# Kernel optimization log

Measured on AMD Instinct MI355X. Metric: run time of the kernel, lower is better.

## Reference

```python
import jax, jax.numpy as jnp
import numpy as np

B, M, D = 64, 256, 256          # batch, tokens, feature dim
A = 18                          # num_actions
E, S = 4, 64                    # num_experts, slots per expert (E*S == M)
H = 512                         # expert hidden size


def setup_inputs() -> dict:
    key = jax.random.key(0)
    ks = jax.random.split(key, 7)
    obs = jax.random.normal(ks[0], (B, M, D), dtype=jnp.float32)
    action = jax.random.randint(ks[1], (B,), 0, A, dtype=jnp.int64)
    # Soft-MoE slot projection phi: [D, E, S]
    phi = jax.random.normal(ks[2], (D, E, S), dtype=jnp.float32) / np.sqrt(D)
    # Per-expert MLP: Dense(H) + relu, then Dense(A*D) output head
    w1 = jax.random.normal(ks[3], (E, D, H), dtype=jnp.float32) * np.sqrt(2.0 / D)
    b1 = jnp.zeros((E, H), dtype=jnp.float32)
    w2 = jax.random.normal(ks[4], (E, H, A * D), dtype=jnp.float32) * np.sqrt(2.0 / H)
    b2 = jnp.zeros((E, A * D), dtype=jnp.float32)
    return {"obs": obs, "action": action, "phi": phi,
            "w1": w1, "b1": b1, "w2": w2, "b2": b2}


def reference(obs, action, phi, w1, b1, w2, b2):
    b, m, d = obs.shape
    # ---- Soft-MoE dispatch / combine (Puigcerver et al.) ----
    logits = jnp.einsum('bmd,des->bmes', obs, phi)            # [b,m,e,s]
    dispatch = jax.nn.softmax(logits, axis=1)                 # softmax over tokens
    combine = jax.nn.softmax(logits.reshape(b, m, E * S), axis=-1)
    combine = combine.reshape(b, m, E, S)                     # softmax over all slots
    slots = jnp.einsum('bmd,bmes->besd', obs, dispatch)       # [b,e,s,d]
    # ---- per-expert MLP: Dense(H)+relu -> Dense(A*d) ----
    h = jax.nn.relu(jnp.einsum('besd,edh->besh', slots, w1) + b1[None, :, None, :])
    y = jnp.einsum('besh,ehk->besk', h, w2) + b2[None, :, None, :]   # k = A*d
    # ---- combine slots back to tokens ----
    out = jnp.einsum('bmes,besk->bmk', combine, y)            # [b,m,A*d]
    # reshape to [b, A, m, d] as in the original module
    out = out.reshape(b, m, A, d).transpose(0, 2, 1, 3)       # [b,A,m,d]
    # ---- one-hot action selection via einsum (as in source) ----
    action_one_hot = jax.nn.one_hot(action, A, dtype=out.dtype)
    logits_out = jnp.einsum('bamd,ba->bmd', out, action_one_hot)
    return logits_out  # logits of the categorical transition distribution
```

## Files before the change

### kernel.cpp

```cpp
#include <hip/hip_runtime.h>

#define B_   64
#define M_   256
#define D_   256
#define A_   18
#define E_   4
#define S_   64
#define ES_  256
#define H_   512
#define K2_  (A_*D_)

typedef _Float16 f16;
typedef _Float16 f16x4 __attribute__((ext_vector_type(4)));
typedef _Float16 f16x8 __attribute__((ext_vector_type(8)));
typedef float    f32x4 __attribute__((ext_vector_type(4)));

static __device__ __forceinline__ f16x8 cat8(f16x4 a, f16x4 b) {
  return __builtin_shufflevector(a, b, 0, 1, 2, 3, 4, 5, 6, 7);
}
static __device__ __forceinline__ f16x8 pack8(float4 u0, float4 u1) {
  f16x8 a;
  a[0] = (f16)u0.x; a[1] = (f16)u0.y; a[2] = (f16)u0.z; a[3] = (f16)u0.w;
  a[4] = (f16)u1.x; a[5] = (f16)u1.y; a[6] = (f16)u1.z; a[7] = (f16)u1.w;
  return a;
}

__global__ __launch_bounds__(256) void k_preplog(
    const float* __restrict__ obs, const float* __restrict__ phi,
    const float* __restrict__ w1, const float* __restrict__ w2,
    const int* __restrict__ action,
    f16* __restrict__ obsT16, f16* __restrict__ w1T, f16* __restrict__ w2T,
    int* __restrict__ order,
    f16* __restrict__ exp16, f16* __restrict__ expT16,
    float* __restrict__ rowpart, float* __restrict__ colpart)
{
  __shared__ f16 Bs[64][264];
  f16 (*T)[68] = reinterpret_cast<f16(*)[68]>(&Bs[0][0]);
  const int bx = blockIdx.x;
  const int t  = threadIdx.x;

  if (bx < 3456) {
    const int rr = t >> 4, cc = (t & 15) * 4;
    const float* src; f16* dst; int R, C, r0, c0;
    if (bx < 1024) {
      const int x = bx & 3, y = (bx >> 2) & 3, z = bx >> 4;
      src = obs + (long)z * (M_ * D_); dst = obsT16 + (long)z * (M_ * D_);
      R = M_; C = D_; r0 = y * 64; c0 = x * 64;
    } else if (bx < 1152) {
      const int idx = bx - 1024;
      const int x = idx & 7, y = (idx >> 3) & 3, z = idx >> 5;
      src = w1 + (long)z * (D_ * H_); dst = w1T + (long)z * (H_ * D_);
      R = D_; C = H_; r0 = y * 64; c0 = x * 64;
    } else {
      const int idx = bx - 1152;
      const int x = idx % 72, rem = idx / 72, y = rem & 7, z = rem >> 3;
      src = w2 + (long)z * ((long)H_ * K2_); dst = w2T + (long)z * ((long)K2_ * H_);
      R = H_; C = K2_; r0 = y * 64; c0 = x * 64;
    }
#pragma unroll
    for (int p = 0; p < 4; ++p) {
      const int row = rr + p * 16;
      const float4 v = *reinterpret_cast<const float4*>(
          &src[(long)(r0 + row) * C + c0 + cc]);
      T[row][cc + 0] = (f16)v.x; T[row][cc + 1] = (f16)v.y;
      T[row][cc + 2] = (f16)v.z; T[row][cc + 3] = (f16)v.w;
    }
    __syncthreads();
#pragma unroll
    for (int p = 0; p < 4; ++p) {
      const int oc = rr + p * 16;
      f16x4 g;
#pragma unroll
      for (int i = 0; i < 4; ++i) g[i] = T[cc + i][oc];
      *reinterpret_cast<f16x4*>(&dst[(long)(c0 + oc) * R + r0 + cc]) = g;
    }
    return;
  }

  if (bx == 3456) {
    if (t < B_) {
      const int a = action[t];
      int rank = 0;
#pragma unroll 8
      for (int i = 0; i < B_; ++i) {
        const int ai = action[i];
        rank += (ai < a) || (ai == a && i < t);
      }
      order[rank] = t;
    }
    return;
  }

  const int lb  = bx - 3457;
  const int es0 = (lb & 3) * 64, m0g = ((lb >> 2) & 3) * 64;
  const int bz  = lb >> 4;
  const long bo = (long)bz * (M_ * D_);
  const long bb = (long)bz * (M_ * ES_);

  {
    const int el = t & 63, wg = t >> 6;
#pragma unroll
    for (int dp = 0; dp < D_; dp += 32) {
      f16x8 hv;
#pragma unroll
      for (int j = 0; j < 8; ++j)
        hv[j] = (f16)phi[(long)(dp + wg * 8 + j) * ES_ + es0 + el];
      *reinterpret_cast<f16x8*>(&Bs[el][dp + wg * 8]) = hv;
    }
  }
  __syncthreads();

  const int w = t >> 6, lane = t & 63;
  const int wr = w >> 1, wc = w & 1;
  const int lr = lane & 15, lk = (lane >> 4) * 8;
  const int orow = (lane >> 4) * 4;

  f32x4 acc[2][2] = {};
  const float* Ap = obs + bo + (long)(m0g + wr * 32 + lr) * D_ + lk;
#pragma unroll
  for (int k0 = 0; k0 < D_; k0 += 32) {
    const float4 u00 = *reinterpret_cast<const float4*>(Ap + k0);
    const float4 u01 = *reinterpret_cast<const float4*>(Ap + k0 + 4);
    const float4 u10 = *reinterpret_cast<const float4*>(Ap + 16 * D_ + k0);
    const float4 u11 = *reinterpret_cast<const float4*>(Ap + 16 * D_ + k0 + 4);
    const f16x8 a0 = pack8(u00, u01);
    const f16x8 a1 = pack8(u10, u11);
    const f16x8 b0 = *reinterpret_cast<const f16x8*>(&Bs[wc * 32 + lr][k0 + lk]);
    const f16x8 b1 = *reinterpret_cast<const f16x8*>(&Bs[wc * 32 + 16 + lr][k0 + lk]);
    acc[0][0] = __builtin_amdgcn_mfma_f32_16x16x32_f16(a0, b0, acc[0][0], 0, 0, 0);
    acc[0][1] = __builtin_amdgcn_mfma_f32_16x16x32_f16(a0, b1, acc[0][1], 0, 0, 0);
    acc[1][0] = __builtin_amdgcn_mfma_f32_16x16x32_f16(a1, b0, acc[1][0], 0, 0, 0);
    acc[1][1] = __builtin_amdgcn_mfma_f32_16x16x32_f16(a1, b1, acc[1][1], 0, 0, 0);
  }
  __syncthreads();

#pragma unroll
  for (int fi = 0; fi < 2; ++fi)
#pragma unroll
    for (int fj = 0; fj < 2; ++fj) {
      const int gm = wr * 32 + fi * 16 + orow;
      const int gn = wc * 32 + fj * 16 + lr;
#pragma unroll
      for (int r = 0; r < 4; ++r)
        T[gm + r][gn] = (f16)__expf(acc[fi][fj][r]);
    }
  __syncthreads();

  {
    const int row = t >> 2, q = t & 3;
    f16x4 p0 = *reinterpret_cast<const f16x4*>(&T[row][q * 16 + 0]);
    f16x4 p1 = *reinterpret_cast<const f16x4*>(&T[row][q * 16 + 4]);
    f16x4 p2 = *reinterpret_cast<const f16x4*>(&T[row][q * 16 + 8]);
    f16x4 p3 = *reinterpret_cast<const f16x4*>(&T[row][q * 16 + 12]);
    f16* dst = exp16 + bb + (long)(m0g + row) * ES_ + es0 + q * 16;
    *reinterpret_cast<f16x8*>(dst)     = cat8(p0, p1);
    *reinterpret_cast<f16x8*>(dst + 8) = cat8(p2, p3);
  }
  {
    const int er = t >> 2, q = t & 3;
    f16x4 g[4];
#pragma unroll
    for (int j = 0; j < 4; ++j)
#pragma unroll
      for (int i = 0; i < 4; ++i)
        g[j][i] = T[q * 16 + j * 4 + i][er];
    f16* dst = expT16 + bb + (long)(es0 + er) * M_ + m0g + q * 16;
    *reinterpret_cast<f16x8*>(dst)     = cat8(g[0], g[1]);
    *reinterpret_cast<f16x8*>(dst + 8) = cat8(g[2], g[3]);
  }
  if (t < 64) {
    float s = 0.f;
#pragma unroll
    for (int i = 0; i < 16; ++i) {
      const f16x4 v = *reinterpret_cast<const f16x4*>(&T[t][i * 4]);
      s += (float)v[0] + (float)v[1] + (float)v[2] + (float)v[3];
    }
    rowpart[((long)bz * 256 + m0g + t) * 4 + (lb & 3)] = s;
  } else if (t < 128) {
    const int es = t - 64;
    float s = 0.f;
#pragma unroll
    for (int i = 0; i < 64; ++i) s += (float)T[i][es];
    colpart[((long)bz * 256 + es0 + es) * 4 + ((lb >> 2) & 3)] = s;
  }
}

#define SPAD 264
#define HPAD2 520
#define MFMA16(a, b, c) __builtin_amdgcn_mfma_f32_16x16x32_f16(a, b, c, 0, 0, 0)

__global__ __launch_bounds__(512, 4) void k_hy5(
    const f16* __restrict__ expT16, const f16* __restrict__ obsT16,
    const float* __restrict__ colpart,
    const f16* __restrict__ w1T, const float* __restrict__ b1,
    const f16* __restrict__ w2T, const float* __restrict__ b2,
    const int* __restrict__ action, const int* __restrict__ order,
    f16* __restrict__ yT16)
{
  __shared__ f16 ss[32][SPAD];
  __shared__ f16 hs[32][HPAD2];
  const int bx = blockIdx.x;
  const int L  = (bx & 7) * 64 + (bx >> 3);
  const int sb = L >> 3, e = (L >> 1) & 3, half = L & 1;
  const int b = order[sb];
  const int s0 = half * 32;
  int a = action[b];
  a = (a < 0) ? 0 : (a >= A_ ? A_ - 1 : a);

  const int t = threadIdx.x, w = t >> 6, lane = t & 63;
  const int lr = lane & 15, lk = (lane >> 4) * 8;
  const int orow = (lane >> 4) * 4;

  const int n0_2 = w * 32;
  const f16* Bp2 = w2T + (long)e * ((long)K2_ * H_)
                 + ((long)a * D_ + n0_2 + lr) * H_ + lk;
  const f16* Bp1 = w1T + (long)e * (H_ * D_) + (long)(w * 64 + lr) * D_ + lk;

  {
    const int n0 = w * 32;
    f32x4 acc00 = {}, acc01 = {}, acc10 = {}, acc11 = {};
    const f16* Ap = expT16 + (long)b * (ES_ * M_)
                  + (long)(e * S_ + s0 + lr) * M_ + lk;
    const f16* Bp = obsT16 + (long)b * (D_ * M_) + (long)(n0 + lr) * M_ + lk;

    f16x8 aq0[4], aq1[4], bq0[4], bq1[4];
#pragma unroll
    for (int p = 0; p < 4; ++p) {
      aq0[p] = *reinterpret_cast<const f16x8*>(Ap + p * 32);
      aq1[p] = *reinterpret_cast<const f16x8*>(Ap + 16 * M_ + p * 32);
      bq0[p] = *reinterpret_cast<const f16x8*>(Bp + p * 32);
      bq1[p] = *reinterpret_cast<const f16x8*>(Bp + 16 * M_ + p * 32);
    }
#pragma unroll
    for (int it = 0; it < 8; ++it) {
      const int c = it & 3;
      const f16x8 a0 = aq0[c], a1 = aq1[c], b0 = bq0[c], b1f = bq1[c];
      if (it < 4) {
        const int k = (it + 4) * 32;
        aq0[c] = *reinterpret_cast<const f16x8*>(Ap + k);
        aq1[c] = *reinterpret_cast<const f16x8*>(Ap + 16 * M_ + k);
        bq0[c] = *reinterpret_cast<const f16x8*>(Bp + k);
        bq1[c] = *reinterpret_cast<const f16x8*>(Bp + 16 * M_ + k);
      }
      acc00 = MFMA16(a0, b0, acc00); acc01 = MFMA16(a0, b1f, acc01);
      acc10 = MFMA16(a1, b0, acc10); acc11 = MFMA16(a1, b1f, acc11);
    }

    f16x8 bq1g[4][4];
#pragma unroll
    for (int p = 0; p < 4; ++p)
#pragma unroll
      for (int fj = 0; fj < 4; ++fj)
        bq1g[p][fj] = *reinterpret_cast<const f16x8*>(
            Bp1 + (long)fj * 16 * D_ + p * 32);

    f32x4 accs[2][2] = {{acc00, acc01}, {acc10, acc11}};
#pragma unroll
    for (int fi = 0; fi < 2; ++fi) {
      float inv[4];
#pragma unroll
      for (int r = 0; r < 4; ++r) {
        const int ges = e * S_ + s0 + fi * 16 + orow + r;
        const float4 cp = *reinterpret_cast<const float4*>(
            &colpart[((long)b * 256 + ges) * 4]);
        inv[r] = 1.0f / (cp.x + cp.y + cp.z + cp.w);
      }
#pragma unroll
      for (int fj = 0; fj < 2; ++fj) {
        const int gm = fi * 16 + orow;
        const int gn = n0 + fj * 16 + lr;
#pragma unroll
        for (int r = 0; r < 4; ++r)
          ss[gm + r][gn] = (f16)(accs[fi][fj][r] * inv[r]);
      }
    }
    __syncthreads();

    {
      const int n1 = w * 64;
      f32x4 acc[2][4] = {};
#pragma unroll
      for (int it = 0; it < 8; ++it) {
        const int c = it & 3;
        f16x8 bf[4];
#pragma unroll
        for (int fj = 0; fj < 4; ++fj) bf[fj] = bq1g[c][fj];
        if (it < 4) {
          const int k = (it + 4) * 32;
#pragma unroll
          for (int fj = 0; fj < 4; ++fj)
            bq1g[c][fj] = *reinterpret_cast<const f16x8*>(
                Bp1 + (long)fj * 16 * D_ + k);
        }
        f16x8 af[2];
#pragma unroll
        for (int fi = 0; fi < 2; ++fi)
          af[fi] = *reinterpret_cast<const f16x8*>(&ss[fi * 16 + lr][it * 32 + lk]);
#pragma unroll
        for (int fi = 0; fi < 2; ++fi)
#pragma unroll
          for (int fj = 0; fj < 4; ++fj)
            acc[fi][fj] = MFMA16(af[fi], bf[fj], acc[fi][fj]);
      }

      f16x8 bq2a[8], bq2b[8];
#pragma unroll
      for (int p = 0; p < 8; ++p) {
        bq2a[p] = *reinterpret_cast<const f16x8*>(Bp2 + p * 32);
        bq2b[p] = *reinterpret_cast<const f16x8*>(Bp2 + 16 * H_ + p * 32);
      }

#pragma unroll
      for (int fi = 0; fi < 2; ++fi)
#pragma unroll
        for (int fj = 0; fj < 4; ++fj) {
          const int gm = fi * 16 + orow;
          const int gn = n1 + fj * 16 + lr;
          const float bv = b1[e * H_ + gn];
#pragma unroll
          for (int r = 0; r < 4; ++r)
            hs[gm + r][gn] = (f16)fmaxf(acc[fi][fj][r] + bv, 0.f);
        }
      __syncthreads();

      {
        f32x4 acc2[2][2] = {};
#pragma unroll
        for (int it = 0; it < 16; ++it) {
          const int c = it & 7;
          const f16x8 b0 = bq2a[c], b1f = bq2b[c];
          if (it < 8) {
            const int k = (it + 8) * 32;
            bq2a[c] = *reinterpret_cast<const f16x8*>(Bp2 + k);
            bq2b[c] = *reinterpret_cast<const f16x8*>(Bp2 + 16 * H_ + k);
          }
          f16x8 af[2];
#pragma unroll
          for (int fi = 0; fi < 2; ++fi)
            af[fi] = *reinterpret_cast<const f16x8*>(&hs[fi * 16 + lr][it * 32 + lk]);
          acc2[0][0] = MFMA16(af[0], b0,  acc2[0][0]);
          acc2[0][1] = MFMA16(af[0], b1f, acc2[0][1]);
          acc2[1][0] = MFMA16(af[1], b0,  acc2[1][0]);
          acc2[1][1] = MFMA16(af[1], b1f, acc2[1][1]);
        }
#pragma unroll
        for (int fi = 0; fi < 2; ++fi)
#pragma unroll
          for (int fj = 0; fj < 2; ++fj) {
            const int gm = fi * 16 + orow;
            const int gn = n0_2 + fj * 16 + lr;
            const float bv = b2[e * K2_ + a * D_ + gn];
            f16x4 h4;
#pragma unroll
            for (int r = 0; r < 4; ++r) h4[r] = (f16)(acc2[fi][fj][r] + bv);
            *reinterpret_cast<f16x4*>(
                &yT16[(long)b * (D_ * ES_) + (long)gn * ES_ + e * S_ + s0 + gm]) = h4;
          }
      }
    }
  }
}

__global__ __launch_bounds__(256) void k_out_s(
    const f16* __restrict__ exp16, const f16* __restrict__ yT16,
    const float* __restrict__ rowpart, float* __restrict__ out)
{
  const int t = threadIdx.x;
  const int w = t >> 6, lane = t & 63;
  const int wr = w >> 1, wc = w & 1;
  const int m0 = blockIdx.y * 64 + wr * 32;
  const int n0 = blockIdx.x * 64 + wc * 32;
  const int lr = lane & 15, lk = (lane >> 4) * 8;
  const long b = blockIdx.z;

  f32x4 acc[2][2] = {};
  const f16* Ap = exp16 + b * (M_ * ES_) + (long)(m0 + lr) * ES_ + lk;
  const f16* Bp = yT16 + b * (D_ * ES_) + (long)(n0 + lr) * ES_ + lk;
#pragma unroll
  for (int k0 = 0; k0 < ES_; k0 += 32) {
    const f16x8 a0 = *reinterpret_cast<const f16x8*>(Ap + k0);
    const f16x8 a1 = *reinterpret_cast<const f16x8*>(Ap + 16 * ES_ + k0);
    const f16x8 b0 = *reinterpret_cast<const f16x8*>(Bp + k0);
    const f16x8 b1 = *reinterpret_cast<const f16x8*>(Bp + 16 * ES_ + k0);
    acc[0][0] = __builtin_amdgcn_mfma_f32_16x16x32_f16(a0, b0, acc[0][0], 0, 0, 0);
    acc[0][1] = __builtin_amdgcn_mfma_f32_16x16x32_f16(a0, b1, acc[0][1], 0, 0, 0);
    acc[1][0] = __builtin_amdgcn_mfma_f32_16x16x32_f16(a1, b0, acc[1][0], 0, 0, 0);
    acc[1][1] = __builtin_amdgcn_mfma_f32_16x16x32_f16(a1, b1, acc[1][1], 0, 0, 0);
  }

  const int orow = (lane >> 4) * 4;
  float* C = out + b * (M_ * D_);
#pragma unroll
  for (int fi = 0; fi < 2; ++fi) {
    float inv[4];
#pragma unroll
    for (int r = 0; r < 4; ++r) {
      const int gm = m0 + fi * 16 + orow + r;
      const float4 rp = *reinterpret_cast<const float4*>(&rowpart[((long)b * 256 + gm) * 4]);
      inv[r] = 1.0f / (rp.x + rp.y + rp.z + rp.w);
    }
#pragma unroll
    for (int fj = 0; fj < 2; ++fj) {
      const int gm = m0 + fi * 16 + orow;
      const int gn = n0 + fj * 16 + lr;
#pragma unroll
      for (int r = 0; r < 4; ++r)
        C[(long)(gm + r) * D_ + gn] = acc[fi][fj][r] * inv[r];
    }
  }
}

extern "C" void kernel_launch(void* const* d_in, const int* in_sizes, int n_in,
                              void* d_out, int out_size, void* d_ws, size_t ws_size,
                              hipStream_t stream)
{
  const float* obs    = (const float*)d_in[0];
  const int*   action = (const int*)d_in[1];
  const float* phi    = (const float*)d_in[2];
  const float* w1     = (const float*)d_in[3];
  const float* b1     = (const float*)d_in[4];
  const float* w2     = (const float*)d_in[5];
  const float* b2     = (const float*)d_in[6];
  float*       out    = (float*)d_out;

  f16* ws = (f16*)d_ws;
  f16* obsT16  = ws + 0;
  f16* w1T     = ws + 4194304;
  f16* w2T     = ws + 4718592;
  f16* exp16   = ws + 14155776;
  f16* expT16  = ws + 18350080;
  f16* yT16    = ws + 22544384;
  float* rowpart = (float*)(ws + 26738688);
  float* colpart = (float*)(ws + 26869760);
  int*   order   = (int*)(ws + 27000832);

  k_preplog<<<dim3(4481),     256, 0, stream>>>(obs, phi, w1, w2, action,
                                                obsT16, w1T, w2T, order,
                                                exp16, expT16, rowpart, colpart);
  k_hy5    <<<dim3(512),      512, 0, stream>>>(expT16, obsT16, colpart,
                                                w1T, b1, w2T, b2,
                                                action, order, yT16);
  k_out_s  <<<dim3(4, 4, 64), 256, 0, stream>>>(exp16, yT16, rowpart, out);
}
```

Before: 102.7 us.

## Stage B operands of expert MLP GEMMs through LDS via direct global-to-LDS loads

```diff
diff --git a/kernel.cpp b/kernel.cpp
--- a/kernel.cpp
+++ b/kernel.cpp
@@ -23,6 +23,12 @@
   a[0] = (f16)u0.x; a[1] = (f16)u0.y; a[2] = (f16)u0.z; a[3] = (f16)u0.w;
   a[4] = (f16)u1.x; a[5] = (f16)u1.y; a[6] = (f16)u1.z; a[7] = (f16)u1.w;
   return a;
+}
+
+typedef const __attribute__((address_space(1))) unsigned int guint;
+typedef __attribute__((address_space(3))) unsigned int luint;
+static __device__ __forceinline__ void gload16(const f16* g, f16* l) {
+  __builtin_amdgcn_global_load_lds((guint*)g, (luint*)l, 16, 0, 0);
 }
 
 __global__ __launch_bounds__(256) void k_preplog(
@@ -189,7 +195,7 @@
 #define HPAD2 520
 #define MFMA16(a, b, c) __builtin_amdgcn_mfma_f32_16x16x32_f16(a, b, c, 0, 0, 0)
 
-__global__ __launch_bounds__(512, 4) void k_hy5(
+__global__ __launch_bounds__(512, 4) void k_hy7(
     const f16* __restrict__ expT16, const f16* __restrict__ obsT16,
     const float* __restrict__ colpart,
     const f16* __restrict__ w1T, const float* __restrict__ b1,
@@ -199,6 +205,9 @@
 {
   __shared__ f16 ss[32][SPAD];
   __shared__ f16 hs[32][HPAD2];
+  f16* ssL = &ss[0][0];
+  f16* hsL = &hs[0][0];
+
   const int bx = blockIdx.x;
   const int L  = (bx & 7) * 64 + (bx >> 3);
   const int sb = L >> 3, e = (L >> 1) & 3, half = L & 1;
@@ -209,52 +218,38 @@
 
   const int t = threadIdx.x, w = t >> 6, lane = t & 63;
   const int lr = lane & 15, lk = (lane >> 4) * 8;
+  const int seg = lane >> 4;
   const int orow = (lane >> 4) * 4;
 
-  const int n0_2 = w * 32;
-  const f16* Bp2 = w2T + (long)e * ((long)K2_ * H_)
-                 + ((long)a * D_ + n0_2 + lr) * H_ + lk;
-  const f16* Bp1 = w1T + (long)e * (H_ * D_) + (long)(w * 64 + lr) * D_ + lk;
-
-  {
+  const f16* srcB0 = obsT16 + (long)b * (D_ * M_);
+  const f16* srcB1 = w1T + (long)e * (H_ * D_);
+  const f16* srcB2 = w2T + (long)e * ((long)K2_ * H_) + (long)a * D_ * H_;
+  const f16* ApG0  = expT16 + (long)b * (ES_ * M_)
+                   + (long)(e * S_ + s0 + lr) * M_ + lk;
+
+  f32x4 acc00 = {}, acc01 = {}, acc10 = {}, acc11 = {};
+#pragma unroll 1
+  for (int kt = 0; kt < 8; ++kt) {
+    __syncthreads();
+#pragma unroll
+    for (int p = 0; p < 2; ++p) {
+      const int j = (w * 2 + p) * 64 + lane;
+      const int row = j >> 2, sg = (j & 3) ^ (row & 3);
+      gload16(srcB0 + (long)row * M_ + kt * 32 + sg * 8, ssL + (w * 2 + p) * 512);
+    }
+    __syncthreads();
+    const f16x8 a0 = *reinterpret_cast<const f16x8*>(ApG0 + kt * 32);
+    const f16x8 a1 = *reinterpret_cast<const f16x8*>(ApG0 + 16 * M_ + kt * 32);
+    const int r0 = w * 32 + lr, r1 = w * 32 + 16 + lr;
+    const f16x8 b0 = *reinterpret_cast<const f16x8*>(&ssL[r0 * 32 + ((seg ^ (r0 & 3)) * 8)]);
+    const f16x8 b1 = *reinterpret_cast<const f16x8*>(&ssL[r1 * 32 + ((seg ^ (r1 & 3)) * 8)]);
+    acc00 = MFMA16(a0, b0, acc00); acc01 = MFMA16(a0, b1, acc01);
+    acc10 = MFMA16(a1, b0, acc10); acc11 = MFMA16(a1, b1, acc11);
+  }
+  __syncthreads();
+  {
+    f32x4 accs[2][2] = {{acc00, acc01}, {acc10, acc11}};
     const int n0 = w * 32;
-    f32x4 acc00 = {}, acc01 = {}, acc10 = {}, acc11 = {};
-    const f16* Ap = expT16 + (long)b * (ES_ * M_)
-                  + (long)(e * S_ + s0 + lr) * M_ + lk;
-    const f16* Bp = obsT16 + (long)b * (D_ * M_) + (long)(n0 + lr) * M_ + lk;
-
-    f16x8 aq0[4], aq1[4], bq0[4], bq1[4];
-#pragma unroll
-    for (int p = 0; p < 4; ++p) {
-      aq0[p] = *reinterpret_cast<const f16x8*>(Ap + p * 32);
-      aq1[p] = *reinterpret_cast<const f16x8*>(Ap + 16 * M_ + p * 32);
-      bq0[p] = *reinterpret_cast<const f16x8*>(Bp + p * 32);
-      bq1[p] = *reinterpret_cast<const f16x8*>(Bp + 16 * M_ + p * 32);
-    }
-#pragma unroll
-    for (int it = 0; it < 8; ++it) {
-      const int c = it & 3;
-      const f16x8 a0 = aq0[c], a1 = aq1[c], b0 = bq0[c], b1f = bq1[c];
-      if (it < 4) {
-        const int k = (it + 4) * 32;
-        aq0[c] = *reinterpret_cast<const f16x8*>(Ap + k);
-        aq1[c] = *reinterpret_cast<const f16x8*>(Ap + 16 * M_ + k);
-        bq0[c] = *reinterpret_cast<const f16x8*>(Bp + k);
-        bq1[c] = *reinterpret_cast<const f16x8*>(Bp + 16 * M_ + k);
-      }
-      acc00 = MFMA16(a0, b0, acc00); acc01 = MFMA16(a0, b1f, acc01);
-      acc10 = MFMA16(a1, b0, acc10); acc11 = MFMA16(a1, b1f, acc11);
-    }
-
-    f16x8 bq1g[4][4];
-#pragma unroll
-    for (int p = 0; p < 4; ++p)
-#pragma unroll
-      for (int fj = 0; fj < 4; ++fj)
-        bq1g[p][fj] = *reinterpret_cast<const f16x8*>(
-            Bp1 + (long)fj * 16 * D_ + p * 32);
-
-    f32x4 accs[2][2] = {{acc00, acc01}, {acc10, acc11}};
 #pragma unroll
     for (int fi = 0; fi < 2; ++fi) {
       float inv[4];
@@ -274,90 +269,94 @@
           ss[gm + r][gn] = (f16)(accs[fi][fj][r] * inv[r]);
       }
     }
+  }
+  __syncthreads();
+
+  f32x4 g1acc[2][4] = {};
+#pragma unroll 1
+  for (int kt = 0; kt < 8; ++kt) {
+    if (kt > 0) __syncthreads();
+#pragma unroll
+    for (int p = 0; p < 4; ++p) {
+      const int j = (w * 4 + p) * 64 + lane;
+      const int row = j >> 2, sg = (j & 3) ^ (row & 3);
+      gload16(srcB1 + (long)row * D_ + kt * 32 + sg * 8, hsL + (w * 4 + p) * 512);
+    }
     __syncthreads();
-
-    {
-      const int n1 = w * 64;
-      f32x4 acc[2][4] = {};
-#pragma unroll
-      for (int it = 0; it < 8; ++it) {
-        const int c = it & 3;
-        f16x8 bf[4];
-#pragma unroll
-        for (int fj = 0; fj < 4; ++fj) bf[fj] = bq1g[c][fj];
-        if (it < 4) {
-          const int k = (it + 4) * 32;
-#pragma unroll
-          for (int fj = 0; fj < 4; ++fj)
-            bq1g[c][fj] = *reinterpret_cast<const f16x8*>(
-                Bp1 + (long)fj * 16 * D_ + k);
-        }
-        f16x8 af[2];
-#pragma unroll
-        for (int fi = 0; fi < 2; ++fi)
-          af[fi] = *reinterpret_cast<const f16x8*>(&ss[fi * 16 + lr][it * 32 + lk]);
-#pragma unroll
-        for (int fi = 0; fi < 2; ++fi)
-#pragma unroll
-          for (int fj = 0; fj < 4; ++fj)
-            acc[fi][fj] = MFMA16(af[fi], bf[fj], acc[fi][fj]);
-      }
-
-      f16x8 bq2a[8], bq2b[8];
-#pragma unroll
-      for (int p = 0; p < 8; ++p) {
-        bq2a[p] = *reinterpret_cast<const f16x8*>(Bp2 + p * 32);
-        bq2b[p] = *reinterpret_cast<const f16x8*>(Bp2 + 16 * H_ + p * 32);
-      }
-
-#pragma unroll
-      for (int fi = 0; fi < 2; ++fi)
-#pragma unroll
-        for (int fj = 0; fj < 4; ++fj) {
-          const int gm = fi * 16 + orow;
-          const int gn = n1 + fj * 16 + lr;
-          const float bv = b1[e * H_ + gn];
-#pragma unroll
-          for (int r = 0; r < 4; ++r)
-            hs[gm + r][gn] = (f16)fmaxf(acc[fi][fj][r] + bv, 0.f);
-        }
+    f16x8 af[2];
+    af[0] = *reinterpret_cast<const f16x8*>(&ss[lr][kt * 32 + lk]);
+    af[1] = *reinterpret_cast<const f16x8*>(&ss[16 + lr][kt * 32 + lk]);
+#pragma unroll
+    for (int fj = 0; fj < 4; ++fj) {
+      const int r = w * 64 + fj * 16 + lr;
+      const f16x8 bf = *reinterpret_cast<const f16x8*>(&hsL[r * 32 + ((seg ^ (r & 3)) * 8)]);
+      g1acc[0][fj] = MFMA16(af[0], bf, g1acc[0][fj]);
+      g1acc[1][fj] = MFMA16(af[1], bf, g1acc[1][fj]);
+    }
+  }
+  __syncthreads();
+
+#pragma unroll
+  for (int p = 0; p < 2; ++p) {
+    const int j = (w * 2 + p) * 64 + lane;
+    const int row = j >> 2, sg = (j & 3) ^ (row & 3);
+    gload16(srcB2 + (long)row * H_ + sg * 8, ssL + (w * 2 + p) * 512);
+  }
+  {
+    const int n1 = w * 64;
+#pragma unroll
+    for (int fi = 0; fi < 2; ++fi)
+#pragma unroll
+      for (int fj = 0; fj < 4; ++fj) {
+        const int gm = fi * 16 + orow;
+        const int gn = n1 + fj * 16 + lr;
+        const float bv = b1[e * H_ + gn];
+#pragma unroll
+        for (int r = 0; r < 4; ++r)
+          hs[gm + r][gn] = (f16)fmaxf(g1acc[fi][fj][r] + bv, 0.f);
+      }
+  }
+  __syncthreads();
+
+  f32x4 acc2[2][2] = {};
+#pragma unroll 1
+  for (int kt = 0; kt < 16; ++kt) {
+    if (kt > 0) {
       __syncthreads();
-
-      {
-        f32x4 acc2[2][2] = {};
-#pragma unroll
-        for (int it = 0; it < 16; ++it) {
-          const int c = it & 7;
-          const f16x8 b0 = bq2a[c], b1f = bq2b[c];
-          if (it < 8) {
-            const int k = (it + 8) * 32;
-            bq2a[c] = *reinterpret_cast<const f16x8*>(Bp2 + k);
-            bq2b[c] = *reinterpret_cast<const f16x8*>(Bp2 + 16 * H_ + k);
-          }
-          f16x8 af[2];
-#pragma unroll
-          for (int fi = 0; fi < 2; ++fi)
-            af[fi] = *reinterpret_cast<const f16x8*>(&hs[fi * 16 + lr][it * 32 + lk]);
-          acc2[0][0] = MFMA16(af[0], b0,  acc2[0][0]);
-          acc2[0][1] = MFMA16(af[0], b1f, acc2[0][1]);
-          acc2[1][0] = MFMA16(af[1], b0,  acc2[1][0]);
-          acc2[1][1] = MFMA16(af[1], b1f, acc2[1][1]);
-        }
-#pragma unroll
-        for (int fi = 0; fi < 2; ++fi)
-#pragma unroll
-          for (int fj = 0; fj < 2; ++fj) {
-            const int gm = fi * 16 + orow;
-            const int gn = n0_2 + fj * 16 + lr;
-            const float bv = b2[e * K2_ + a * D_ + gn];
-            f16x4 h4;
-#pragma unroll
-            for (int r = 0; r < 4; ++r) h4[r] = (f16)(acc2[fi][fj][r] + bv);
-            *reinterpret_cast<f16x4*>(
-                &yT16[(long)b * (D_ * ES_) + (long)gn * ES_ + e * S_ + s0 + gm]) = h4;
-          }
-      }
-    }
+#pragma unroll
+      for (int p = 0; p < 2; ++p) {
+        const int j = (w * 2 + p) * 64 + lane;
+        const int row = j >> 2, sg = (j & 3) ^ (row & 3);
+        gload16(srcB2 + (long)row * H_ + kt * 32 + sg * 8, ssL + (w * 2 + p) * 512);
+      }
+      __syncthreads();
+    }
+    f16x8 af[2];
+    af[0] = *reinterpret_cast<const f16x8*>(&hs[lr][kt * 32 + lk]);
+    af[1] = *reinterpret_cast<const f16x8*>(&hs[16 + lr][kt * 32 + lk]);
+#pragma unroll
+    for (int fj = 0; fj < 2; ++fj) {
+      const int r = w * 32 + fj * 16 + lr;
+      const f16x8 bf = *reinterpret_cast<const f16x8*>(&ssL[r * 32 + ((seg ^ (r & 3)) * 8)]);
+      acc2[0][fj] = MFMA16(af[0], bf, acc2[0][fj]);
+      acc2[1][fj] = MFMA16(af[1], bf, acc2[1][fj]);
+    }
+  }
+  {
+    const int n0_2 = w * 32;
+#pragma unroll
+    for (int fi = 0; fi < 2; ++fi)
+#pragma unroll
+      for (int fj = 0; fj < 2; ++fj) {
+        const int gm = fi * 16 + orow;
+        const int gn = n0_2 + fj * 16 + lr;
+        const float bv = b2[e * K2_ + a * D_ + gn];
+        f16x4 h4;
+#pragma unroll
+        for (int r = 0; r < 4; ++r) h4[r] = (f16)(acc2[fi][fj][r] + bv);
+        *reinterpret_cast<f16x4*>(
+            &yT16[(long)b * (D_ * ES_) + (long)gn * ES_ + e * S_ + s0 + gm]) = h4;
+      }
   }
 }
 
@@ -437,7 +436,7 @@
   k_preplog<<<dim3(4481),     256, 0, stream>>>(obs, phi, w1, w2, action,
                                                 obsT16, w1T, w2T, order,
                                                 exp16, expT16, rowpart, colpart);
-  k_hy5    <<<dim3(512),      512, 0, stream>>>(expT16, obsT16, colpart,
+  k_hy7    <<<dim3(512),      512, 0, stream>>>(expT16, obsT16, colpart,
                                                 w1T, b1, w2T, b2,
                                                 action, order, yT16);
   k_out_s  <<<dim3(4, 4, 64), 256, 0, stream>>>(exp16, yT16, rowpart, out);
```

Result: faster. 92.28 us (-10.2%).
